# Kernel optimization log

Measured on AMD Instinct MI355X. Metric: run time of the kernel, lower is better.

Reference implementation:

```python
import jax, jax.numpy as jnp
import numpy as np

B, S, D = 4, 4096, 1024

def setup_inputs() -> dict:
    key = jax.random.key(0)
    k1, k2, k3 = jax.random.split(key, 3)
    scale = 1.0 / np.sqrt(D)
    x = jax.random.normal(k1, (B, S, D), dtype=jnp.float32)
    W_qkv = jax.random.normal(k2, (3 * D, D), dtype=jnp.float32) * scale
    b_qkv = jnp.zeros((3 * D,), dtype=jnp.float32)
    W_gate = jax.random.normal(k3, (D, D), dtype=jnp.float32) * scale
    b_gate = jnp.zeros((D,), dtype=jnp.float32)
    return {"x": x, "W_qkv": W_qkv, "b_qkv": b_qkv, "W_gate": W_gate, "b_gate": b_gate}

def reference(x, W_qkv, b_qkv, W_gate, b_gate):
    # qkv projection: [B,S,3D]
    qkv = jnp.einsum('bsd,ed->bse', x, W_qkv) + b_qkv
    q, k, v = jnp.split(qkv, 3, axis=-1)  # each [B,S,D]
    # associative linear-attention state: running sum of k*v along seq
    kv_state = jnp.cumsum(k * v, axis=1)
    g = jax.nn.sigmoid(jnp.einsum('bsd,ed->bse', x, W_gate) + b_gate)
    return q * kv_state * g
```

## Files before the change

kernel.cpp:

```cpp
#include <hip/hip_runtime.h>
#include <hip/hip_bf16.h>

#define BB 4
#define SS 4096
#define DD 1024
#define MM (BB * SS)
#define KK DD
#define NN (4 * DD)

typedef __attribute__((ext_vector_type(8))) short bf16x8;
typedef __attribute__((ext_vector_type(4))) float f32x4;

__device__ __forceinline__ unsigned short f2bf(float f) {
  unsigned u = __float_as_uint(f);
  u += 0x7FFF + ((u >> 16) & 1);
  return (unsigned short)(u >> 16);
}
__device__ __forceinline__ float bf2f(unsigned short h) {
  return __uint_as_float(((unsigned)h) << 16);
}

__global__ __launch_bounds__(256) void k_convert(const float* __restrict__ src,
                                                 unsigned short* __restrict__ dst, int n4) {
  int i = blockIdx.x * blockDim.x + threadIdx.x;
  int stride = gridDim.x * blockDim.x;
  for (; i < n4; i += stride) {
    float4 v = reinterpret_cast<const float4*>(src)[i];
    ushort4 o;
    o.x = f2bf(v.x); o.y = f2bf(v.y); o.z = f2bf(v.z); o.w = f2bf(v.w);
    reinterpret_cast<ushort4*>(dst)[i] = o;
  }
}

__global__ __launch_bounds__(256) void k_convert_wperm(const float* __restrict__ Wqkv,
                                                       const float* __restrict__ Wgate,
                                                       unsigned short* __restrict__ dst) {
  int n = blockIdx.x;
  const float* src;
  if (n < 1024) {
    src = Wqkv + (size_t)n * 1024;
  } else if (n < 3072) {
    int t = (n - 1024) >> 4;
    int d = ((t >> 1) << 4) + (n & 15);
    src = Wqkv + (size_t)(1024 + ((t & 1) << 10) + d) * 1024;
  } else {
    src = Wgate + (size_t)(n - 3072) * 1024;
  }
  unsigned short* o = dst + (size_t)n * 1024;
  int i = threadIdx.x * 4;
  float4 v = *(const float4*)(src + i);
  ushort4 u;
  u.x = f2bf(v.x); u.y = f2bf(v.y); u.z = f2bf(v.z); u.w = f2bf(v.w);
  *(ushort4*)(o + i) = u;
}

#define VMW4() asm volatile("s_waitcnt vmcnt(4)" ::: "memory")
#define VMW0() asm volatile("s_waitcnt vmcnt(0)" ::: "memory")

__global__ __launch_bounds__(512, 2) void k_gemm3(const unsigned short* __restrict__ A,
                                                  const unsigned short* __restrict__ W,
                                                  unsigned short* __restrict__ Qd,
                                                  unsigned short* __restrict__ KVd,
                                                  unsigned short* __restrict__ Gd,
                                                  const float* __restrict__ bqkv,
                                                  const float* __restrict__ bgate) {
  __shared__ unsigned short sm[65536];

  int bid0 = blockIdx.x;
  int bid = (bid0 & 7) * 128 + (bid0 >> 3);
  int tn = bid & 15, tm = bid >> 4;
  int m0 = tm * 256, n0 = tn * 256;

  int tid = threadIdx.x, wave = tid >> 6, lane = tid & 63;
  int wm = wave >> 2, wn = wave & 3;
  int r = lane & 15, g = lane >> 4;

  int pt = tid * 16;
  int psw = pt ^ (((pt >> 9) & 1) << 5);
  int srow = psw >> 7;
  int scol = (psw & 127) >> 1;
  const unsigned short* Ag = A + (size_t)(m0 + srow) * KK + scol;
  const unsigned short* Wg = W + (size_t)(n0 + srow) * KK + scol;

#define STG_A(kt, h, d) do {                                                              \
    __builtin_amdgcn_global_load_lds(                                                     \
        (const __attribute__((address_space(1))) void*)(Ag + (size_t)(h)*131072 + (kt)*64), \
        (__attribute__((address_space(3))) void*)&sm[(d)*16384 + (h)*8192 + wave*512], 16, 0, 0); \
    __builtin_amdgcn_global_load_lds(                                                     \
        (const __attribute__((address_space(1))) void*)(Ag + (size_t)(h)*131072 + 65536 + (kt)*64), \
        (__attribute__((address_space(3))) void*)&sm[(d)*16384 + (h)*8192 + 4096 + wave*512], 16, 0, 0); \
  } while (0)
#define STG_B(kt, h, d) do {                                                              \
    __builtin_amdgcn_global_load_lds(                                                     \
        (const __attribute__((address_space(1))) void*)(Wg + (size_t)(h)*131072 + (kt)*64), \
        (__attribute__((address_space(3))) void*)&sm[32768 + (d)*16384 + (h)*8192 + wave*512], 16, 0, 0); \
    __builtin_amdgcn_global_load_lds(                                                     \
        (const __attribute__((address_space(1))) void*)(Wg + (size_t)(h)*131072 + 65536 + (kt)*64), \
        (__attribute__((address_space(3))) void*)&sm[32768 + (d)*16384 + (h)*8192 + 4096 + wave*512], 16, 0, 0); \
  } while (0)

  int sx = ((r >> 2) & 1) << 4;
  int aRd = (wm * 8192 + r * 64 + g * 8) ^ sx;
  int bRd = (32768 + (wn >> 1) * 8192 + (wn & 1) * 4096 + r * 64 + g * 8) ^ sx;

#define LDSA(d, m, ks) (*reinterpret_cast<const bf16x8*>(&sm[aRd + (d)*16384 + (m)*1024 + (ks)*32]))
#define LDSB(d, n, ks) (*reinterpret_cast<const bf16x8*>(&sm[bRd + (d)*16384 + (n)*1024 + (ks)*32]))

  f32x4 acc[8][4] = {};
  bf16x8 a[4][2], Bn[4][2];

#define RD_A(d, mb) do { _Pragma("unroll") for (int mi = 0; mi < 4; ++mi) {               \
    _Pragma("unroll") for (int ks = 0; ks < 2; ++ks) { a[mi][ks] = LDSA(d, (mb)+mi, ks); } } } while (0)
#define RD_B(d, nb) do { _Pragma("unroll") for (int ni = 0; ni < 2; ++ni) {               \
    _Pragma("unroll") for (int ks = 0; ks < 2; ++ks) { Bn[(nb)+ni][ks] = LDSB(d, (nb)+ni, ks); } } } while (0)

#define BARW() do { __builtin_amdgcn_s_barrier();                                         \
    asm volatile("s_waitcnt lgkmcnt(0)" ::: "memory");                                    \
    __builtin_amdgcn_sched_barrier(0); } while (0)
#define ENDB() __builtin_amdgcn_s_barrier()

#define MFMA16(mb, nb) do {                                                               \
    __builtin_amdgcn_s_setprio(1);                                                        \
    _Pragma("unroll") for (int mi = 0; mi < 4; ++mi) {                                    \
      _Pragma("unroll") for (int ni = 0; ni < 2; ++ni) {                                  \
        _Pragma("unroll") for (int ks = 0; ks < 2; ++ks) {                                \
          acc[(mb)+mi][(nb)+ni] = __builtin_amdgcn_mfma_f32_16x16x32_bf16(                \
              a[mi][ks], Bn[(nb)+ni][ks], acc[(mb)+mi][(nb)+ni], 0, 0, 0);                \
        } } }                                                                             \
    __builtin_amdgcn_s_setprio(0); } while (0)

  STG_A(0, 0, 0); STG_A(0, 1, 0);
  STG_B(0, 0, 0); STG_B(0, 1, 0);
  STG_B(1, 0, 1); STG_B(1, 1, 1);
  VMW4();
  __builtin_amdgcn_s_barrier();

  for (int i = 0; i < 7; ++i) {
    int tb = 2 * i + 1, tc = 2 * i + 2, td = 2 * i + 3;
    RD_A(0, 0); RD_B(0, 0); STG_A(tb, 0, 1);
    BARW(); MFMA16(0, 0); ENDB();
    RD_B(0, 2); STG_A(tb, 1, 1);
    BARW(); MFMA16(0, 2); ENDB();
    RD_A(0, 4); STG_B(tc, 0, 0);
    BARW(); MFMA16(4, 0); ENDB();
    STG_B(tc, 1, 0);
    BARW(); MFMA16(4, 2); VMW4(); ENDB();
    RD_A(1, 0); RD_B(1, 0); STG_A(tc, 0, 0);
    BARW(); MFMA16(0, 0); ENDB();
    RD_B(1, 2); STG_A(tc, 1, 0);
    BARW(); MFMA16(0, 2); ENDB();
    RD_A(1, 4); STG_B(td, 0, 1);
    BARW(); MFMA16(4, 0); ENDB();
    STG_B(td, 1, 1);
    BARW(); MFMA16(4, 2); VMW4(); ENDB();
  }
  RD_A(0, 0); RD_B(0, 0); STG_A(15, 0, 1);
  BARW(); MFMA16(0, 0); ENDB();
  RD_B(0, 2); STG_A(15, 1, 1);
  BARW(); MFMA16(0, 2); ENDB();
  RD_A(0, 4);
  BARW(); MFMA16(4, 0); ENDB();
  BARW(); MFMA16(4, 2); VMW0(); ENDB();
  RD_A(1, 0); RD_B(1, 0);
  BARW(); MFMA16(0, 0); ENDB();
  RD_B(1, 2);
  BARW(); MFMA16(0, 2); ENDB();
  RD_A(1, 4);
  BARW(); MFMA16(4, 0); ENDB();
  BARW(); MFMA16(4, 2);

  int growb = m0 + wm * 128 + g * 4;
  if (tn < 4) {
#pragma unroll
    for (int n = 0; n < 4; ++n) {
      int col = n0 + wn * 64 + n * 16 + r;
      float bias = bqkv[col];
#pragma unroll
      for (int m = 0; m < 8; ++m)
#pragma unroll
        for (int q = 0; q < 4; ++q)
          Qd[(size_t)(growb + m * 16 + q) * DD + col] = f2bf(acc[m][n][q] + bias);
    }
  } else if (tn < 12) {
    int cb = n0 - 1024 + wn * 64;
#pragma unroll
    for (int np = 0; np < 2; ++np) {
      int d = (cb >> 1) + np * 16 + r;
      float bk = bqkv[1024 + d], bv = bqkv[2048 + d];
#pragma unroll
      for (int m = 0; m < 8; ++m)
#pragma unroll
        for (int q = 0; q < 4; ++q) {
          float kvv = (acc[m][2 * np][q] + bk) * (acc[m][2 * np + 1][q] + bv);
          KVd[(size_t)(growb + m * 16 + q) * DD + d] = f2bf(kvv);
        }
    }
  } else {
    int cb0 = n0 - 3072;
#pragma unroll
    for (int n = 0; n < 4; ++n) {
      int c = cb0 + wn * 64 + n * 16 + r;
      float bias = bgate[c];
#pragma unroll
      for (int m = 0; m < 8; ++m)
#pragma unroll
        for (int q = 0; q < 4; ++q) {
          float gv = acc[m][n][q] + bias;
          Gd[(size_t)(growb + m * 16 + q) * DD + c] = f2bf(1.f / (1.f + __expf(-gv)));
        }
    }
  }
#undef STG_A
#undef STG_B
#undef LDSA
#undef LDSB
#undef RD_A
#undef RD_B
#undef BARW
#undef ENDB
#undef MFMA16
}

#define NCH 128
#define CSZ (SS / NCH)

__global__ __launch_bounds__(256) void k_pass1(const unsigned short* __restrict__ KV,
                                               float* __restrict__ part) {
  int b = blockIdx.x >> 7;
  int c = blockIdx.x & (NCH - 1);
  int d = threadIdx.x * 4;
  float a0 = 0.f, a1 = 0.f, a2 = 0.f, a3 = 0.f;
  for (int s = c * CSZ; s < (c + 1) * CSZ; ++s) {
    ushort4 kv = *(const ushort4*)&KV[(size_t)(b * SS + s) * DD + d];
    a0 += bf2f(kv.x); a1 += bf2f(kv.y); a2 += bf2f(kv.z); a3 += bf2f(kv.w);
  }
  float4 o = {a0, a1, a2, a3};
  *(float4*)&part[(size_t)(b * NCH + c) * DD + d] = o;
}

__global__ __launch_bounds__(256) void k_pass3(const unsigned short* __restrict__ Q,
                                               const unsigned short* __restrict__ KV,
                                               const unsigned short* __restrict__ G,
                                               const float* __restrict__ part,
                                               float* __restrict__ out) {
  int b = blockIdx.x >> 7;
  int c = blockIdx.x & (NCH - 1);
  int d = threadIdx.x * 4;
  float4 a = {0.f, 0.f, 0.f, 0.f};
  const float* pb = &part[(size_t)b * NCH * DD + d];
  for (int cc = 0; cc < c; ++cc) {
    float4 p = *(const float4*)(pb + (size_t)cc * DD);
    a.x += p.x; a.y += p.y; a.z += p.z; a.w += p.w;
  }
  for (int s = c * CSZ; s < (c + 1) * CSZ; ++s) {
    size_t rowb = (size_t)(b * SS + s) * DD;
    ushort4 q4 = *(const ushort4*)&Q[rowb + d];
    ushort4 kv4 = *(const ushort4*)&KV[rowb + d];
    ushort4 g4 = *(const ushort4*)&G[rowb + d];
    a.x += bf2f(kv4.x); a.y += bf2f(kv4.y); a.z += bf2f(kv4.z); a.w += bf2f(kv4.w);
    float4 o;
    o.x = bf2f(q4.x) * a.x * bf2f(g4.x);
    o.y = bf2f(q4.y) * a.y * bf2f(g4.y);
    o.z = bf2f(q4.z) * a.z * bf2f(g4.z);
    o.w = bf2f(q4.w) * a.w * bf2f(g4.w);
    *(float4*)&out[rowb + d] = o;
  }
}

extern "C" void kernel_launch(void* const* d_in, const int* in_sizes, int n_in,
                              void* d_out, int out_size, void* d_ws, size_t ws_size,
                              hipStream_t stream) {
  const float* x = (const float*)d_in[0];
  const float* Wqkv = (const float*)d_in[1];
  const float* bqkv = (const float*)d_in[2];
  const float* Wgate = (const float*)d_in[3];
  const float* bgate = (const float*)d_in[4];
  float* out = (float*)d_out;

  char* ws = (char*)d_ws;
  unsigned short* xb = (unsigned short*)ws;
  unsigned short* wb = (unsigned short*)(ws + (size_t)33554432);
  unsigned short* Qd = (unsigned short*)(ws + (size_t)41943040);
  unsigned short* KVd = (unsigned short*)(ws + (size_t)75497472);
  unsigned short* Gd = (unsigned short*)(ws + (size_t)109051904);
  float* part = (float*)(ws + (size_t)142606336);

  k_convert<<<2048, 256, 0, stream>>>(x, xb, MM * KK / 4);
  k_convert_wperm<<<4096, 256, 0, stream>>>(Wqkv, Wgate, wb);

  k_gemm3<<<1024, 512, 0, stream>>>(xb, wb, Qd, KVd, Gd, bqkv, bgate);

  k_pass1<<<BB * NCH, 256, 0, stream>>>(KVd, part);
  k_pass3<<<BB * NCH, 256, 0, stream>>>(Qd, KVd, Gd, part, out);
}
```

Baseline: 337.7 us.

## Fuse chunk partial sums into GEMM epilogue, merge convert kernels, widen LDS swizzle

The per-chunk kv partial sums are now reduced inside the GEMM epilogue with cross-lane shuffles and written directly to the partials buffer. This removes the separate pass that re-read the whole KV tensor. The two fp32-to-bf16 conversion kernels are merged into one launch, and the LDS XOR swizzle now spans 8 rows instead of 2 to reduce bank conflicts on the MFMA operand reads. The trade-off is extra epilogue work and shuffles in the GEMM. The partial sums are taken from fp32 values rather than the rounded bf16 values that are stored.

```diff
diff --git a/kernel.cpp b/kernel.cpp
--- a/kernel.cpp
+++ b/kernel.cpp
@@ -20,38 +20,41 @@
   return __uint_as_float(((unsigned)h) << 16);
 }
 
-__global__ __launch_bounds__(256) void k_convert(const float* __restrict__ src,
-                                                 unsigned short* __restrict__ dst, int n4) {
-  int i = blockIdx.x * blockDim.x + threadIdx.x;
-  int stride = gridDim.x * blockDim.x;
-  for (; i < n4; i += stride) {
-    float4 v = reinterpret_cast<const float4*>(src)[i];
-    ushort4 o;
-    o.x = f2bf(v.x); o.y = f2bf(v.y); o.z = f2bf(v.z); o.w = f2bf(v.w);
-    reinterpret_cast<ushort4*>(dst)[i] = o;
-  }
-}
-
-__global__ __launch_bounds__(256) void k_convert_wperm(const float* __restrict__ Wqkv,
-                                                       const float* __restrict__ Wgate,
-                                                       unsigned short* __restrict__ dst) {
-  int n = blockIdx.x;
-  const float* src;
-  if (n < 1024) {
-    src = Wqkv + (size_t)n * 1024;
-  } else if (n < 3072) {
-    int t = (n - 1024) >> 4;
-    int d = ((t >> 1) << 4) + (n & 15);
-    src = Wqkv + (size_t)(1024 + ((t & 1) << 10) + d) * 1024;
+__global__ __launch_bounds__(256) void k_prep(const float* __restrict__ x,
+                                              const float* __restrict__ Wqkv,
+                                              const float* __restrict__ Wgate,
+                                              unsigned short* __restrict__ xb,
+                                              unsigned short* __restrict__ wb) {
+  int blk = blockIdx.x;
+  if (blk < 4096) {
+    int n = blk;
+    const float* src;
+    if (n < 1024) {
+      src = Wqkv + (size_t)n * 1024;
+    } else if (n < 3072) {
+      int t = (n - 1024) >> 4;
+      int d = ((t >> 1) << 4) + (n & 15);
+      src = Wqkv + (size_t)(1024 + ((t & 1) << 10) + d) * 1024;
+    } else {
+      src = Wgate + (size_t)(n - 3072) * 1024;
+    }
+    unsigned short* o = wb + (size_t)n * 1024;
+    int i = threadIdx.x * 4;
+    float4 v = *(const float4*)(src + i);
+    ushort4 u;
+    u.x = f2bf(v.x); u.y = f2bf(v.y); u.z = f2bf(v.z); u.w = f2bf(v.w);
+    *(ushort4*)(o + i) = u;
   } else {
-    src = Wgate + (size_t)(n - 3072) * 1024;
-  }
-  unsigned short* o = dst + (size_t)n * 1024;
-  int i = threadIdx.x * 4;
-  float4 v = *(const float4*)(src + i);
-  ushort4 u;
-  u.x = f2bf(v.x); u.y = f2bf(v.y); u.z = f2bf(v.z); u.w = f2bf(v.w);
-  *(ushort4*)(o + i) = u;
+    int i0 = (blk - 4096) * 1024 + threadIdx.x;
+#pragma unroll
+    for (int it = 0; it < 4; ++it) {
+      int i = i0 + it * 256;
+      float4 v = reinterpret_cast<const float4*>(x)[i];
+      ushort4 u;
+      u.x = f2bf(v.x); u.y = f2bf(v.y); u.z = f2bf(v.z); u.w = f2bf(v.w);
+      reinterpret_cast<ushort4*>(xb)[i] = u;
+    }
+  }
 }
 
 #define VMW4() asm volatile("s_waitcnt vmcnt(4)" ::: "memory")
@@ -62,6 +65,7 @@
                                                   unsigned short* __restrict__ Qd,
                                                   unsigned short* __restrict__ KVd,
                                                   unsigned short* __restrict__ Gd,
+                                                  float* __restrict__ part,
                                                   const float* __restrict__ bqkv,
                                                   const float* __restrict__ bgate) {
   __shared__ unsigned short sm[65536];
@@ -76,7 +80,7 @@
   int r = lane & 15, g = lane >> 4;
 
   int pt = tid * 16;
-  int psw = pt ^ (((pt >> 9) & 1) << 5);
+  int psw = pt ^ (((pt >> 7) & 7) << 4);
   int srow = psw >> 7;
   int scol = (psw & 127) >> 1;
   const unsigned short* Ag = A + (size_t)(m0 + srow) * KK + scol;
@@ -99,12 +103,14 @@
         (__attribute__((address_space(3))) void*)&sm[32768 + (d)*16384 + (h)*8192 + 4096 + wave*512], 16, 0, 0); \
   } while (0)
 
-  int sx = ((r >> 2) & 1) << 4;
-  int aRd = (wm * 8192 + r * 64 + g * 8) ^ sx;
-  int bRd = (32768 + (wn >> 1) * 8192 + (wn & 1) * 4096 + r * 64 + g * 8) ^ sx;
-
-#define LDSA(d, m, ks) (*reinterpret_cast<const bf16x8*>(&sm[aRd + (d)*16384 + (m)*1024 + (ks)*32]))
-#define LDSB(d, n, ks) (*reinterpret_cast<const bf16x8*>(&sm[bRd + (d)*16384 + (n)*1024 + (ks)*32]))
+  int sx = (r & 7) << 3;
+  int aX0 = (r * 64 + g * 8) ^ sx;
+  int aX1 = (r * 64 + 32 + g * 8) ^ sx;
+  int aReg = wm * 8192;
+  int bReg = 32768 + (wn >> 1) * 8192 + (wn & 1) * 4096;
+
+#define LDSA(d, m, ks) (*reinterpret_cast<const bf16x8*>(&sm[aReg + (d)*16384 + (m)*1024 + ((ks) ? aX1 : aX0)]))
+#define LDSB(d, n, ks) (*reinterpret_cast<const bf16x8*>(&sm[bReg + (d)*16384 + (n)*1024 + ((ks) ? aX1 : aX0)]))
 
   f32x4 acc[8][4] = {};
   bf16x8 a[4][2], Bn[4][2];
@@ -182,18 +188,33 @@
           Qd[(size_t)(growb + m * 16 + q) * DD + col] = f2bf(acc[m][n][q] + bias);
     }
   } else if (tn < 12) {
-    int cb = n0 - 1024 + wn * 64;
+    int dbase = ((n0 - 1024) >> 1) + (wn * 32);
 #pragma unroll
     for (int np = 0; np < 2; ++np) {
-      int d = (cb >> 1) + np * 16 + r;
+      int d = dbase + np * 16 + r;
       float bk = bqkv[1024 + d], bv = bqkv[2048 + d];
-#pragma unroll
-      for (int m = 0; m < 8; ++m)
+      float pairsum = 0.f;
+#pragma unroll
+      for (int m = 0; m < 8; ++m) {
+        float ps = 0.f;
 #pragma unroll
         for (int q = 0; q < 4; ++q) {
           float kvv = (acc[m][2 * np][q] + bk) * (acc[m][2 * np + 1][q] + bv);
           KVd[(size_t)(growb + m * 16 + q) * DD + d] = f2bf(kvv);
+          ps += kvv;
         }
+        ps += __shfl_xor(ps, 16, 64);
+        ps += __shfl_xor(ps, 32, 64);
+        if ((m & 1) == 0) {
+          pairsum = ps;
+        } else {
+          pairsum += ps;
+          if (lane < 16) {
+            int cg = tm * 8 + wm * 4 + (m >> 1);
+            part[(size_t)cg * DD + d] = pairsum;
+          }
+        }
+      }
     }
   } else {
     int cb0 = n0 - 3072;
@@ -223,20 +244,6 @@
 
 #define NCH 128
 #define CSZ (SS / NCH)
-
-__global__ __launch_bounds__(256) void k_pass1(const unsigned short* __restrict__ KV,
-                                               float* __restrict__ part) {
-  int b = blockIdx.x >> 7;
-  int c = blockIdx.x & (NCH - 1);
-  int d = threadIdx.x * 4;
-  float a0 = 0.f, a1 = 0.f, a2 = 0.f, a3 = 0.f;
-  for (int s = c * CSZ; s < (c + 1) * CSZ; ++s) {
-    ushort4 kv = *(const ushort4*)&KV[(size_t)(b * SS + s) * DD + d];
-    a0 += bf2f(kv.x); a1 += bf2f(kv.y); a2 += bf2f(kv.z); a3 += bf2f(kv.w);
-  }
-  float4 o = {a0, a1, a2, a3};
-  *(float4*)&part[(size_t)(b * NCH + c) * DD + d] = o;
-}
 
 __global__ __launch_bounds__(256) void k_pass3(const unsigned short* __restrict__ Q,
                                                const unsigned short* __restrict__ KV,
@@ -285,11 +292,7 @@
   unsigned short* Gd = (unsigned short*)(ws + (size_t)109051904);
   float* part = (float*)(ws + (size_t)142606336);
 
-  k_convert<<<2048, 256, 0, stream>>>(x, xb, MM * KK / 4);
-  k_convert_wperm<<<4096, 256, 0, stream>>>(Wqkv, Wgate, wb);
-
-  k_gemm3<<<1024, 512, 0, stream>>>(xb, wb, Qd, KVd, Gd, bqkv, bgate);
-
-  k_pass1<<<BB * NCH, 256, 0, stream>>>(KVd, part);
+  k_prep<<<8192, 256, 0, stream>>>(x, Wqkv, Wgate, xb, wb);
+  k_gemm3<<<1024, 512, 0, stream>>>(xb, wb, Qd, KVd, Gd, part, bqkv, bgate);
   k_pass3<<<BB * NCH, 256, 0, stream>>>(Qd, KVd, Gd, part, out);
 }
```

Result: faster. 319.9 us (-5.3%).
